# Performance work log

Hardware: AMD Instinct MI355X
Metric: run time of the kernel (lower is better)

## Reference

```python
import jax, jax.numpy as jnp
import numpy as np

H = 256       # hidden_size
W2V = 300     # word embedding dim
POS = 30      # pos embedding dim
NF = 100      # filters per n-gram CNN
VOCAB = 50000
NPOS = 100
N_EDUS = 1024
L = 20        # tokens per EDU


def setup_inputs() -> dict:
    key = jax.random.key(0)
    ks = jax.random.split(key, 22)
    def nrm(k, shape, s=0.05):
        return jax.random.normal(k, shape, dtype=jnp.float32) * s
    cw = W2V + POS  # CNN input width = 330
    # valid transition sequence: S, then (S, R) repeated n-1 times -> 2n-1 steps
    transes = jnp.concatenate([jnp.zeros((1,), jnp.int32),
                               jnp.tile(jnp.array([0, 1], jnp.int32), N_EDUS - 1)])
    return {
        "edu_words": jax.random.randint(ks[0], (N_EDUS, L), 0, VOCAB),
        "edu_poses": jax.random.randint(ks[1], (N_EDUS, L), 0, NPOS),
        "transes": transes,
        "word_emb": nrm(ks[2], (VOCAB, W2V), 1.0),
        "pos_emb": nrm(ks[3], (NPOS, POS), 1.0),
        "Wu": nrm(ks[4], (NF, 1, 1, cw)), "bu": nrm(ks[5], (NF,)),
        "Wb": nrm(ks[6], (NF, 1, 2, cw)), "bb": nrm(ks[7], (NF,)),
        "Wt": nrm(ks[8], (NF, 1, 3, cw)), "bt": nrm(ks[9], (NF,)),
        "Wp": nrm(ks[10], (2 * H, 2 * W2V + POS + 3 * NF)), "bp": nrm(ks[11], (2 * H,)),
        "Wih": nrm(ks[12], (4 * H, 3 * H)), "Whh": nrm(ks[13], (4 * H, H)),
        "bih": nrm(ks[14], (4 * H,)), "bhh": nrm(ks[15], (4 * H,)),
        "Wc": nrm(ks[16], (5 * H, 3 * H)), "bc": nrm(ks[17], (5 * H,)),
        "Ws": nrm(ks[18], (2, H)), "bs": nrm(ks[19], (2,)),
    }


def _encode_edus(edu_words, edu_poses, word_emb, pos_emb, Wu, bu, Wb, bb, Wt, bt, Wp, bp):
    we = word_emb[edu_words]                # [N, L, 300]
    pe = pos_emb[edu_poses]                 # [N, L, 30]
    x = jnp.concatenate([we, pe], axis=-1)[:, None, :, :]  # NCHW [N,1,L,330]
    def conv_pool(W, b, pad):
        # kernel spans full width -> output width 1; pad only along time
        y = jax.lax.conv_general_dilated(x, W, (1, 1), ((pad, pad), (0, 0)),
                                         dimension_numbers=("NCHW", "OIHW", "NCHW"))[..., 0]
        return jax.nn.relu(y + b[None, :, None]).max(axis=-1)  # [N, F]
    feats = jnp.concatenate([we[:, 0], we[:, -1], pe[:, 0],
                             conv_pool(Wu, bu, 0), conv_pool(Wb, bb, 1),
                             conv_pool(Wt, bt, 2)], axis=-1)   # [N, 930]
    h, c = jnp.split(feats @ Wp.T + bp, 2, axis=-1)
    return h, c


def _parse_loss(edu_words, edu_poses, transes, word_emb, pos_emb, Wu, bu, Wb, bb, Wt, bt,
                Wp, bp, Wih, Whh, bih, bhh, Wc, bc, Ws, bs):
    eh, ec = _encode_edus(edu_words, edu_poses, word_emb, pos_emb, Wu, bu, Wb, bb, Wt, bt, Wp, bp)
    M = N_EDUS + 2
    buf_h = jnp.concatenate([eh, jnp.zeros((2, H), jnp.float32)], axis=0)
    buf_c = jnp.concatenate([ec, jnp.zeros((2, H), jnp.float32)], axis=0)
    stack_h = jnp.zeros((M, H), jnp.float32)  # slots 0,1 are the initial placeholders
    stack_c = jnp.zeros((M, H), jnp.float32)

    def lstm(xv, h, c):  # torch LSTMCell gate order i,f,g,o
        g = xv @ Wih.T + bih + h @ Whh.T + bhh
        i, f, gg, o = jnp.split(g, 4)
        c2 = jax.nn.sigmoid(f) * c + jax.nn.sigmoid(i) * jnp.tanh(gg)
        return jax.nn.sigmoid(o) * jnp.tanh(c2), c2

    def track(sh, sptr, bptr, th, tc):
        xv = jnp.concatenate([sh[sptr - 1], sh[sptr - 2], buf_h[bptr]])
        return lstm(xv, th, tc)

    sptr = jnp.int32(2)
    bptr = jnp.int32(0)
    th, tc = track(stack_h, sptr, bptr, jnp.zeros(H, jnp.float32), jnp.zeros(H, jnp.float32))

    def step(carry, trans):
        sh, sc, sptr, bptr, th, tc = carry
        logits = th @ Ws.T + bs  # scorer MLP with mlp_layers=1 -> single Linear
        is_shift = trans == 0
        # SHIFT candidate: push buffer front
        sh_s = sh.at[sptr].set(buf_h[bptr])
        sc_s = sc.at[sptr].set(buf_c[bptr])
        # REDUCE candidate: tree-LSTM composition of top two stack items
        h1, c1 = sh[sptr - 1], sc[sptr - 1]
        h2, c2 = sh[sptr - 2], sc[sptr - 2]
        g = jnp.concatenate([h1, h2, th]) @ Wc.T + bc
        a, i, f1, f2, o = jnp.split(g, 5)
        rc = jnp.tanh(a) * jax.nn.sigmoid(i) + jax.nn.sigmoid(f1) * c1 + jax.nn.sigmoid(f2) * c2
        rh = jax.nn.sigmoid(o) * jnp.tanh(rc)
        sh_r = sh.at[sptr - 2].set(rh)
        sc_r = sc.at[sptr - 2].set(rc)
        sh2 = jnp.where(is_shift, sh_s, sh_r)
        sc2 = jnp.where(is_shift, sc_s, sc_r)
        sptr2 = jnp.where(is_shift, sptr + 1, sptr - 1)
        bptr2 = jnp.where(is_shift, bptr + 1, bptr)
        th2, tc2 = track(sh2, sptr2, bptr2, th, tc)
        return (sh2, sc2, sptr2, bptr2, th2, tc2), logits

    _, pred = jax.lax.scan(step, (stack_h, stack_c, sptr, bptr, th, tc), transes)
    logp = jax.nn.log_softmax(pred, axis=-1)
    return -jnp.mean(logp[jnp.arange(transes.shape[0]), transes])


def reference(edu_words, edu_poses, transes, word_emb, pos_emb, Wu, bu, Wb, bb, Wt, bt,
              Wp, bp, Wih, Whh, bih, bhh, Wc, bc, Ws, bs):
    return _parse_loss(edu_words, edu_poses, transes, word_emb, pos_emb, Wu, bu, Wb, bb,
                       Wt, bt, Wp, bp, Wih, Whh, bih, bhh, Wc, bc, Ws, bs)
```

## Files before the change

kernel.cpp:

```cpp
#include <hip/hip_runtime.h>
#include <math.h>

#define NEDU  1024
#define LTOK  20
#define CW    330
#define HDIM  256
#define FEAT  930
#define MSLOT 1026
#define NWG   64

#define O_WCATT 0
#define SZ_WCATT (330*600)
#define O_F     (O_WCATT + SZ_WCATT)
#define SZ_F    (NEDU*FEAT)
#define O_BUFH  (O_F + SZ_F)
#define SZ_BUF  (MSLOT*HDIM)
#define O_BUFC  (O_BUFH + SZ_BUF)
#define O_STKT  (O_BUFC + SZ_BUF)
#define O_THT   (O_STKT + MSLOT*HDIM)
#define O_RHT   (O_THT + 2*HDIM)
#define O_LOSSP (O_RHT + HDIM)
#define NZERO   ((MSLOT + 3) * HDIM)

#define AG __HIP_MEMORY_SCOPE_AGENT
__device__ __forceinline__ unsigned long long aload64(const unsigned long long* p) {
  return __hip_atomic_load(p, __ATOMIC_RELAXED, AG);
}
__device__ __forceinline__ void astore(unsigned* p, unsigned v) {
  __hip_atomic_store(p, v, __ATOMIC_RELAXED, AG);
}
__device__ __forceinline__ unsigned tagbits(float v, unsigned ver) {
  return (__float_as_uint(v) & ~3u) | (ver & 3u);
}
__device__ __forceinline__ float sigm(float x) { return 1.f / (1.f + expf(-x)); }

__device__ __forceinline__ void sync_lds() {
  asm volatile("s_waitcnt lgkmcnt(0)\n\ts_barrier" ::: "memory");
}

__device__ __forceinline__ void gather1T(const unsigned* base, int lane, unsigned tag,
                                         float* x) {
  const unsigned long long* p = (const unsigned long long*)base + 2 * lane;
  for (int it = 0;; ++it) {
    const unsigned long long a = aload64(p), b = aload64(p + 1);
    const bool ok = (((unsigned)a & 3u) == tag) & (((unsigned)(a >> 32) & 3u) == tag) &
                    (((unsigned)b & 3u) == tag) & (((unsigned)(b >> 32) & 3u) == tag);
    if (__ballot(ok) == ~0ull) {
      x[0] = __uint_as_float((unsigned)a); x[1] = __uint_as_float((unsigned)(a >> 32));
      x[2] = __uint_as_float((unsigned)b); x[3] = __uint_as_float((unsigned)(b >> 32));
      return;
    }
    if (it > 48) __builtin_amdgcn_s_sleep(1);
  }
}
__device__ __forceinline__ void gather2T(const unsigned* b1, unsigned t1,
                                         const unsigned* b2, unsigned t2,
                                         int lane, float* x1, float* x2) {
  const unsigned long long* p1 = (const unsigned long long*)b1 + 2 * lane;
  const unsigned long long* p2 = (const unsigned long long*)b2 + 2 * lane;
  for (int it = 0;; ++it) {
    const unsigned long long a = aload64(p1), b = aload64(p1 + 1);
    const unsigned long long c = aload64(p2), d = aload64(p2 + 1);
    const bool ok = (((unsigned)a & 3u) == t1) & (((unsigned)(a >> 32) & 3u) == t1) &
                    (((unsigned)b & 3u) == t1) & (((unsigned)(b >> 32) & 3u) == t1) &
                    (((unsigned)c & 3u) == t2) & (((unsigned)(c >> 32) & 3u) == t2) &
                    (((unsigned)d & 3u) == t2) & (((unsigned)(d >> 32) & 3u) == t2);
    if (__ballot(ok) == ~0ull) {
      x1[0] = __uint_as_float((unsigned)a); x1[1] = __uint_as_float((unsigned)(a >> 32));
      x1[2] = __uint_as_float((unsigned)b); x1[3] = __uint_as_float((unsigned)(b >> 32));
      x2[0] = __uint_as_float((unsigned)c); x2[1] = __uint_as_float((unsigned)(c >> 32));
      x2[2] = __uint_as_float((unsigned)d); x2[3] = __uint_as_float((unsigned)(d >> 32));
      return;
    }
    if (it > 48) __builtin_amdgcn_s_sleep(1);
  }
}

__global__ void prep_kernel(const float* __restrict__ Wu, const float* __restrict__ Wb,
                            const float* __restrict__ Wt, float* __restrict__ ws) {
  const int i0 = blockIdx.x * blockDim.x + threadIdx.x;
  const int st = gridDim.x * blockDim.x;
  for (int i = i0; i < SZ_WCATT; i += st) {
    const int k = i / 600, c = i - 600 * k;
    float v;
    if (c < 100)      v = Wu[c * 330 + k];
    else if (c < 300) { const int q = c - 100; v = Wb[(q % 100) * 660 + (q / 100) * 330 + k]; }
    else              { const int q = c - 300; v = Wt[(q % 100) * 990 + (q / 100) * 330 + k]; }
    ws[O_WCATT + i] = v;
  }
  unsigned* z = (unsigned*)ws + O_STKT;
  for (int i = i0; i < NZERO; i += st) z[i] = 0u;
  for (int i = i0; i < 2 * HDIM; i += st) {
    ws[O_BUFH + NEDU * HDIM + i] = 0.f;
    ws[O_BUFC + NEDU * HDIM + i] = 0.f;
  }
}

__global__ __launch_bounds__(256) void encode_kernel(
    const int* __restrict__ edu_words, const int* __restrict__ edu_poses,
    const float* __restrict__ word_emb, const float* __restrict__ pos_emb,
    const float* __restrict__ bu, const float* __restrict__ bb,
    const float* __restrict__ bt, float* __restrict__ ws) {
  __shared__ __align__(16) float xlT[CW * LTOK];
  __shared__ float zl[300 * 21];
  __shared__ float convout[300];
  const int n = blockIdx.x, tid = threadIdx.x;
  const float* WcatT = ws + O_WCATT;

  for (int i = tid; i < LTOK * CW; i += 256) {
    const int l = i / CW, k = i - l * CW;
    float v;
    if (k < 300) v = word_emb[(size_t)edu_words[n * LTOK + l] * 300 + k];
    else         v = pos_emb[(size_t)edu_poses[n * LTOK + l] * 30 + (k - 300)];
    xlT[k * LTOK + l] = v;
  }
  __syncthreads();

  for (int f = tid; f < 300; f += 256) {
    float acc[LTOK];
#pragma unroll
    for (int l = 0; l < LTOK; ++l) acc[l] = 0.f;
    for (int k = 0; k < CW; ++k) {
      const float w = WcatT[k * 600 + f];
      const float4* xp = (const float4*)(xlT + k * LTOK);
      union { float4 v[5]; float s[20]; } xu;
      xu.v[0] = xp[0]; xu.v[1] = xp[1]; xu.v[2] = xp[2]; xu.v[3] = xp[3]; xu.v[4] = xp[4];
#pragma unroll
      for (int l = 0; l < LTOK; ++l) acc[l] += w * xu.s[l];
    }
#pragma unroll
    for (int l = 0; l < LTOK; ++l) zl[f * 21 + l] = acc[l];
  }
  __syncthreads();
  if (tid < 200) {
    float m;
    if (tid < 100) {
      const int f = tid; const float b = bu[f];
      m = zl[f * 21] + b;
      for (int l = 1; l < 20; ++l) m = fmaxf(m, zl[f * 21 + l] + b);
    } else {
      const int f = tid - 100; const float b = bb[f];
      const float* z0 = zl + (100 + f) * 21;
      const float* z1 = zl + (200 + f) * 21;
      m = z1[0] + b;
      for (int u = 1; u <= 19; ++u) m = fmaxf(m, z0[u - 1] + z1[u] + b);
      m = fmaxf(m, z0[19] + b);
    }
    convout[tid] = fmaxf(m, 0.f);
  }
  __syncthreads();

  for (int f = tid; f < 300; f += 256) {
    float acc[LTOK];
#pragma unroll
    for (int l = 0; l < LTOK; ++l) acc[l] = 0.f;
    for (int k = 0; k < CW; ++k) {
      const float w = WcatT[k * 600 + 300 + f];
      const float4* xp = (const float4*)(xlT + k * LTOK);
      union { float4 v[5]; float s[20]; } xu;
      xu.v[0] = xp[0]; xu.v[1] = xp[1]; xu.v[2] = xp[2]; xu.v[3] = xp[3]; xu.v[4] = xp[4];
#pragma unroll
      for (int l = 0; l < LTOK; ++l) acc[l] += w * xu.s[l];
    }
#pragma unroll
    for (int l = 0; l < LTOK; ++l) zl[f * 21 + l] = acc[l];
  }
  __syncthreads();
  if (tid < 100) {
    const int f = tid; const float b = bt[f];
    const float* z0 = zl + f * 21;
    const float* z1 = zl + (100 + f) * 21;
    const float* z2 = zl + (200 + f) * 21;
    float m = z2[0] + b;
    m = fmaxf(m, z1[0] + z2[1] + b);
    for (int u = 2; u <= 19; ++u) m = fmaxf(m, z0[u - 2] + z1[u - 1] + z2[u] + b);
    m = fmaxf(m, z0[18] + z1[19] + b);
    m = fmaxf(m, z0[19] + b);
    convout[200 + f] = fmaxf(m, 0.f);
  }
  __syncthreads();

  float* Fr = ws + O_F + (size_t)n * FEAT;
  for (int j = tid; j < FEAT; j += 256) {
    float v;
    if (j < 300)      v = xlT[j * LTOK + 0];
    else if (j < 600) v = xlT[(j - 300) * LTOK + 19];
    else if (j < 630) v = xlT[(j - 300) * LTOK + 0];
    else              v = convout[j - 630];
    Fr[j] = v;
  }
}

__global__ __launch_bounds__(256) void proj_kernel(const float* __restrict__ Wp,
                                                   const float* __restrict__ bp,
                                                   float* __restrict__ ws) {
  __shared__ float As[64][17];
  __shared__ float Bs[64][17];
  const float* F = ws + O_F;
  float* bufh = ws + O_BUFH;
  float* bufc = ws + O_BUFC;
  const int tid = threadIdx.x;
  const int m0 = blockIdx.x * 64, n0 = blockIdx.y * 64;
  const int mm0 = (tid & 15) * 4, nn0 = (tid >> 4) * 4;
  float acc[4][4] = {{0.f}};
  for (int k0 = 0; k0 < FEAT; k0 += 16) {
    for (int i = tid; i < 64 * 16; i += 256) {
      const int mm = i >> 4, kk = i & 15;
      const int gk = k0 + kk;
      As[mm][kk] = (gk < FEAT) ? F[(size_t)(m0 + mm) * FEAT + gk] : 0.f;
      Bs[mm][kk] = (gk < FEAT) ? Wp[(size_t)(n0 + mm) * FEAT + gk] : 0.f;
    }
    __syncthreads();
#pragma unroll
    for (int kk = 0; kk < 16; ++kk) {
      float av[4], bv[4];
#pragma unroll
      for (int i = 0; i < 4; ++i) av[i] = As[mm0 + i][kk];
#pragma unroll
      for (int j = 0; j < 4; ++j) bv[j] = Bs[nn0 + j][kk];
#pragma unroll
      for (int i = 0; i < 4; ++i)
#pragma unroll
        for (int j = 0; j < 4; ++j) acc[i][j] += av[i] * bv[j];
    }
    __syncthreads();
  }
#pragma unroll
  for (int i = 0; i < 4; ++i) {
    const int m = m0 + mm0 + i;
#pragma unroll
    for (int j = 0; j < 4; ++j) {
      const int nn = n0 + nn0 + j;
      const float v = acc[i][j] + bp[nn];
      if (nn < 256) bufh[(size_t)m * 256 + nn] = v;
      else          bufc[(size_t)m * 256 + (nn - 256)] = v;
    }
  }
}

__global__ __launch_bounds__(256, 1) void parse_kernel(
    const int* __restrict__ transes, int nT,
    const float* __restrict__ Wih, const float* __restrict__ Whh,
    const float* __restrict__ bih, const float* __restrict__ bhh,
    const float* __restrict__ Wc, const float* __restrict__ bc,
    const float* __restrict__ Wsc, float* __restrict__ ws) {
  const int tid = threadIdx.x;
  const int lane = tid & 63;
  const int wv = tid >> 6;
  const int bx = blockIdx.x;
  const int j0 = bx * 4;

  const float* bufh = ws + O_BUFH;
  const float* bufc = ws + O_BUFC;
  unsigned* stkT = (unsigned*)ws + O_STKT;
  unsigned* thT  = (unsigned*)ws + O_THT;
  unsigned* rhT  = (unsigned*)ws + O_RHT;
  float* lossp   = ws + O_LOSSP;

  __shared__ float sc_lds[MSLOT][4];
  __shared__ unsigned vstk[MSLOT];
  __shared__ float tc_lds[2][4];
  __shared__ float g_lds[20];
  __shared__ float rh_st[4];
  __shared__ float part_lds[8];

  float wt[4][16]; float bt_[4];
#pragma unroll
  for (int q = 0; q < 4; ++q) {
    const int rg = wv * 256 + j0 + q;
#pragma unroll
    for (int blk = 0; blk < 3; ++blk) {
      const float4 w = *(const float4*)(Wih + (size_t)rg * 768 + blk * 256 + 4 * lane);
      wt[q][4 * blk + 0] = w.x; wt[q][4 * blk + 1] = w.y;
      wt[q][4 * blk + 2] = w.z; wt[q][4 * blk + 3] = w.w;
    }
    const float4 wh = *(const float4*)(Whh + (size_t)rg * 256 + 4 * lane);
    wt[q][12] = wh.x; wt[q][13] = wh.y; wt[q][14] = wh.z; wt[q][15] = wh.w;
    bt_[q] = bih[rg] + bhh[rg];
  }
  float wcm[5][12]; float bc_[5];
#pragma unroll
  for (int q = 0; q < 5; ++q) {
    const int row = 5 * wv + q, gate = row >> 2, jj = row & 3;
    const int rg = gate * 256 + j0 + jj;
#pragma unroll
    for (int blk = 0; blk < 3; ++blk) {
      const float4 w = *(const float4*)(Wc + (size_t)rg * 768 + blk * 256 + 4 * lane);
      wcm[q][4 * blk + 0] = w.x; wcm[q][4 * blk + 1] = w.y;
      wcm[q][4 * blk + 2] = w.z; wcm[q][4 * blk + 3] = w.w;
    }
    bc_[q] = bc[rg];
  }
  float ws0 = 0.f, ws1 = 0.f;
  if (tid < 4) { ws0 = Wsc[j0 + tid]; ws1 = Wsc[256 + j0 + tid]; }

  for (int i = tid; i < MSLOT; i += 256) vstk[i] = 0u;
  if (tid < 4) { sc_lds[0][tid] = 0.f; sc_lds[1][tid] = 0.f;
                 tc_lds[0][tid] = 0.f; tc_lds[1][tid] = 0.f; }
  __syncthreads();

  unsigned V = 0, vrh = 0;
  int sptr = 2, bptr = 0;

  auto red4 = [&](float& a0, float& a1, float& a2, float& a3) {
#pragma unroll
    for (int off = 32; off; off >>= 1) {
      a0 += __shfl_down(a0, off, 64); a1 += __shfl_down(a1, off, 64);
      a2 += __shfl_down(a2, off, 64); a3 += __shfl_down(a3, off, 64);
    }
  };
  auto red5 = [&](float& a0, float& a1, float& a2, float& a3, float& a4) {
#pragma unroll
    for (int off = 32; off; off >>= 1) {
      a0 += __shfl_down(a0, off, 64); a1 += __shfl_down(a1, off, 64);
      a2 += __shfl_down(a2, off, 64); a3 += __shfl_down(a3, off, 64);
      a4 += __shfl_down(a4, off, 64);
    }
  };

  auto fin_track = [&]() {
    const int j = j0 + tid;
    const float gi = g_lds[tid], gf = g_lds[4 + tid], gg = g_lds[8 + tid], go = g_lds[12 + tid];
    const float cn = sigm(gf) * tc_lds[V & 1][tid] + sigm(gi) * tanhf(gg);
    tc_lds[(V + 1) & 1][tid] = cn;
    const float th = sigm(go) * tanhf(cn);
    astore(thT + ((V + 1) & 1) * HDIM + j, tagbits(th, V + 1));
    part_lds[tid] = ws0 * th; part_lds[4 + tid] = ws1 * th;
  };
  auto emit_loss = [&]() {
    float* lp = lossp + (size_t)V * 128 + bx * 2;
    lp[0] = part_lds[0] + part_lds[1] + part_lds[2] + part_lds[3];
    lp[1] = part_lds[4] + part_lds[5] + part_lds[6] + part_lds[7];
  };
  auto dyn_track = [&](const unsigned* fbase, unsigned ftag, int fblk,
                       float s0, float s1, float s2, float s3) {
    float x[4];
    gather1T(fbase, lane, ftag, x);
    float d0 = 0.f, d1 = 0.f, d2 = 0.f, d3 = 0.f;
#pragma unroll
    for (int c = 0; c < 4; ++c) {
      d0 += wt[0][4 * fblk + c] * x[c]; d1 += wt[1][4 * fblk + c] * x[c];
      d2 += wt[2][4 * fblk + c] * x[c]; d3 += wt[3][4 * fblk + c] * x[c];
    }
    red4(d0, d1, d2, d3);
    if (lane == 0) {
      g_lds[wv * 4 + 0] = s0 + d0 + bt_[0]; g_lds[wv * 4 + 1] = s1 + d1 + bt_[1];
      g_lds[wv * 4 + 2] = s2 + d2 + bt_[2]; g_lds[wv * 4 + 3] = s3 + d3 + bt_[3];
    }
    sync_lds();
    if (tid < 4) fin_track();
    if (tid == 0) emit_loss();
  };

  {
    float p1[4], p2[4];
    gather2T(stkT + HDIM, 0u, stkT, 0u, lane, p1, p2);
    const float4 f3 = *(const float4*)(bufh + 4 * lane);
    const float p3[4] = { f3.x, f3.y, f3.z, f3.w };
    float s0 = 0.f, s1 = 0.f, s2 = 0.f, s3 = 0.f;
#pragma unroll
    for (int c = 0; c < 4; ++c) {
      s0 += wt[0][c] * p1[c] + wt[0][4 + c] * p2[c] + wt[0][8 + c] * p3[c];
      s1 += wt[1][c] * p1[c] + wt[1][4 + c] * p2[c] + wt[1][8 + c] * p3[c];
      s2 += wt[2][c] * p1[c] + wt[2][4 + c] * p2[c] + wt[2][8 + c] * p3[c];
      s3 += wt[3][c] * p1[c] + wt[3][4 + c] * p2[c] + wt[3][8 + c] * p3[c];
    }
    red4(s0, s1, s2, s3);
    dyn_track(thT + (V & 1) * HDIM, V & 3, 3, s0, s1, s2, s3);
    sync_lds();
    V += 1;
  }

  for (int t = 0; t < nT; ++t) {
    const int tr = transes[t];
    if (tr) {
      {
        float h1[4], h2[4];
        gather2T(stkT + (size_t)(sptr - 1) * HDIM, vstk[sptr - 1] & 3,
                 stkT + (size_t)(sptr - 2) * HDIM, vstk[sptr - 2] & 3, lane, h1, h2);
        float s0 = 0.f, s1 = 0.f, s2 = 0.f, s3 = 0.f, s4 = 0.f;
#pragma unroll
        for (int c = 0; c < 4; ++c) {
          s0 += wcm[0][c] * h1[c] + wcm[0][4 + c] * h2[c];
          s1 += wcm[1][c] * h1[c] + wcm[1][4 + c] * h2[c];
          s2 += wcm[2][c] * h1[c] + wcm[2][4 + c] * h2[c];
          s3 += wcm[3][c] * h1[c] + wcm[3][4 + c] * h2[c];
          s4 += wcm[4][c] * h1[c] + wcm[4][4 + c] * h2[c];
        }
        red5(s0, s1, s2, s3, s4);
        float x[4];
        gather1T(thT + (V & 1) * HDIM, lane, V & 3, x);
        float d0 = 0.f, d1 = 0.f, d2 = 0.f, d3 = 0.f, d4 = 0.f;
#pragma unroll
        for (int c = 0; c < 4; ++c) {
          d0 += wcm[0][8 + c] * x[c]; d1 += wcm[1][8 + c] * x[c];
          d2 += wcm[2][8 + c] * x[c]; d3 += wcm[3][8 + c] * x[c];
          d4 += wcm[4][8 + c] * x[c];
        }
        red5(d0, d1, d2, d3, d4);
        if (lane == 0) {
          g_lds[5 * wv + 0] = s0 + d0 + bc_[0]; g_lds[5 * wv + 1] = s1 + d1 + bc_[1];
          g_lds[5 * wv + 2] = s2 + d2 + bc_[2]; g_lds[5 * wv + 3] = s3 + d3 + bc_[3];
          g_lds[5 * wv + 4] = s4 + d4 + bc_[4];
        }
      }
      sync_lds();
      if (tid < 4) {
        const int j = j0 + tid;
        const float ga = g_lds[tid], gi = g_lds[4 + tid], gf1 = g_lds[8 + tid],
                    gf2 = g_lds[12 + tid], go = g_lds[16 + tid];
        const float c1 = sc_lds[sptr - 1][tid];
        const float c2 = sc_lds[sptr - 2][tid];
        const float rc = tanhf(ga) * sigm(gi) + sigm(gf1) * c1 + sigm(gf2) * c2;
        const float rh = sigm(go) * tanhf(rc);
        sc_lds[sptr - 2][tid] = rc;
        rh_st[tid] = rh;
        astore(rhT + j, tagbits(rh, vrh + 1));
      }
      sync_lds();
      vrh += 1;

      {
        const int slot = sptr - 2;
        const unsigned nv = vstk[slot] + 1;
        if (tid < 4)
          astore(stkT + (size_t)slot * HDIM + j0 + tid, tagbits(rh_st[tid], nv));
        float p2[4], xth[4];
        gather2T(stkT + (size_t)(sptr - 3) * HDIM, vstk[sptr - 3] & 3,
                 thT + (V & 1) * HDIM, V & 3, lane, p2, xth);
        const float4 f3 = *(const float4*)(bufh + (size_t)bptr * HDIM + 4 * lane);
        const float p3[4] = { f3.x, f3.y, f3.z, f3.w };
        float s0 = 0.f, s1 = 0.f, s2 = 0.f, s3 = 0.f;
#pragma unroll
        for (int c = 0; c < 4; ++c) {
          s0 += wt[0][4 + c] * p2[c] + wt[0][8 + c] * p3[c] + wt[0][12 + c] * xth[c];
          s1 += wt[1][4 + c] * p2[c] + wt[1][8 + c] * p3[c] + wt[1][12 + c] * xth[c];
          s2 += wt[2][4 + c] * p2[c] + wt[2][8 + c] * p3[c] + wt[2][12 + c] * xth[c];
          s3 += wt[3][4 + c] * p2[c] + wt[3][8 + c] * p3[c] + wt[3][12 + c] * xth[c];
        }
        red4(s0, s1, s2, s3);
        dyn_track(rhT, vrh & 3, 0, s0, s1, s2, s3);
        if (tid == 0) vstk[slot] = nv;
        sync_lds();
        V += 1; sptr -= 1;
      }
    } else {
      const unsigned nv = vstk[sptr] + 1;
      if (tid < 4) {
        const int j = j0 + tid;
        astore(stkT + (size_t)sptr * HDIM + j, tagbits(bufh[(size_t)bptr * HDIM + j], nv));
        sc_lds[sptr][tid] = bufc[(size_t)bptr * HDIM + j];
      }
      const float4 f1 = *(const float4*)(bufh + (size_t)bptr * HDIM + 4 * lane);
      const float4 f3 = *(const float4*)(bufh + (size_t)(bptr + 1) * HDIM + 4 * lane);
      float p2[4];
      gather1T(stkT + (size_t)(sptr - 1) * HDIM, lane, vstk[sptr - 1] & 3, p2);
      const float p1[4] = { f1.x, f1.y, f1.z, f1.w };
      const float p3[4] = { f3.x, f3.y, f3.z, f3.w };
      float s0 = 0.f, s1 = 0.f, s2 = 0.f, s3 = 0.f;
#pragma unroll
      for (int c = 0; c < 4; ++c) {
        s0 += wt[0][c] * p1[c] + wt[0][4 + c] * p2[c] + wt[0][8 + c] * p3[c];
        s1 += wt[1][c] * p1[c] + wt[1][4 + c] * p2[c] + wt[1][8 + c] * p3[c];
        s2 += wt[2][c] * p1[c] + wt[2][4 + c] * p2[c] + wt[2][8 + c] * p3[c];
        s3 += wt[3][c] * p1[c] + wt[3][4 + c] * p2[c] + wt[3][8 + c] * p3[c];
      }
      red4(s0, s1, s2, s3);
      dyn_track(thT + (V & 1) * HDIM, V & 3, 3, s0, s1, s2, s3);
      if (tid == 0) vstk[sptr] = nv;
      sync_lds();
      V += 1; sptr += 1; bptr += 1;
    }
  }
}

__global__ __launch_bounds__(256) void loss_kernel(const int* __restrict__ transes, int nT,
                                                   const float* __restrict__ bsc,
                                                   const float* __restrict__ ws,
                                                   float* __restrict__ out) {
  const int tid = threadIdx.x;
  const float* lossp = ws + O_LOSSP;
  __shared__ double red[256];
  double acc = 0.0;
  for (int t = tid; t < nT; t += 256) {
    const float* lp = lossp + (size_t)t * 128;
    float a0 = 0.f, a1 = 0.f;
    for (int w = 0; w < 64; ++w) { a0 += lp[2 * w]; a1 += lp[2 * w + 1]; }
    const float l0 = a0 + bsc[0], l1 = a1 + bsc[1];
    const float mx = fmaxf(l0, l1);
    acc += (double)(mx + logf(expf(l0 - mx) + expf(l1 - mx)) - (transes[t] ? l1 : l0));
  }
  red[tid] = acc;
  __syncthreads();
  for (int s = 128; s; s >>= 1) {
    if (tid < s) red[tid] += red[tid + s];
    __syncthreads();
  }
  if (tid == 0) out[0] = (float)(red[0] / (double)nT);
}

extern "C" void kernel_launch(void* const* d_in, const int* in_sizes, int n_in,
                              void* d_out, int out_size, void* d_ws, size_t ws_size,
                              hipStream_t stream) {
  const int*   edu_words = (const int*)d_in[0];
  const int*   edu_poses = (const int*)d_in[1];
  const int*   transes   = (const int*)d_in[2];
  const float* word_emb  = (const float*)d_in[3];
  const float* pos_emb   = (const float*)d_in[4];
  const float* Wu  = (const float*)d_in[5];
  const float* bu  = (const float*)d_in[6];
  const float* Wb  = (const float*)d_in[7];
  const float* bb  = (const float*)d_in[8];
  const float* Wt  = (const float*)d_in[9];
  const float* bt  = (const float*)d_in[10];
  const float* Wp  = (const float*)d_in[11];
  const float* bp  = (const float*)d_in[12];
  const float* Wih = (const float*)d_in[13];
  const float* Whh = (const float*)d_in[14];
  const float* bih = (const float*)d_in[15];
  const float* bhh = (const float*)d_in[16];
  const float* Wc  = (const float*)d_in[17];
  const float* bc  = (const float*)d_in[18];
  const float* Wsc = (const float*)d_in[19];
  const float* bsc = (const float*)d_in[20];
  float* ws  = (float*)d_ws;
  float* out = (float*)d_out;
  int nT = in_sizes[2];

  hipLaunchKernelGGL(prep_kernel, dim3(256), dim3(256), 0, stream, Wu, Wb, Wt, ws);
  hipLaunchKernelGGL(encode_kernel, dim3(NEDU), dim3(256), 0, stream,
                     edu_words, edu_poses, word_emb, pos_emb, bu, bb, bt, ws);
  hipLaunchKernelGGL(proj_kernel, dim3(16, 8), dim3(256), 0, stream, Wp, bp, ws);

  void* args[] = { (void*)&transes, (void*)&nT, (void*)&Wih, (void*)&Whh, (void*)&bih,
                   (void*)&bhh, (void*)&Wc, (void*)&bc, (void*)&Wsc, (void*)&ws };
  hipLaunchCooperativeKernel((const void*)parse_kernel, dim3(NWG), dim3(256), args, 0, stream);

  hipLaunchKernelGGL(loss_kernel, dim3(1), dim3(256), 0, stream, transes, nT, bsc, ws, out);
}
```

Baseline: 7.515 ms.

## Make each wavefront own one hidden unit, removing intra-block barriers in parse loop

After: 13.01 ms. 73.1% more time.

```diff
diff --git a/kernel.cpp b/kernel.cpp
--- a/kernel.cpp
+++ b/kernel.cpp
@@ -9,21 +9,25 @@
 #define MSLOT 1026
 #define NWG   64
 
+typedef unsigned long long u64;
+
 #define O_WCATT 0
 #define SZ_WCATT (330*600)
 #define O_F     (O_WCATT + SZ_WCATT)
 #define SZ_F    (NEDU*FEAT)
-#define O_BUFH  (O_F + SZ_F)
+#define O_LOSSP O_F
+#define SZ_LOSSP (2048*512)
+#define SZ_FL   1048576
+#define O_BUFH  (O_F + SZ_FL)
 #define SZ_BUF  (MSLOT*HDIM)
 #define O_BUFC  (O_BUFH + SZ_BUF)
 #define O_STKT  (O_BUFC + SZ_BUF)
 #define O_THT   (O_STKT + MSLOT*HDIM)
 #define O_RHT   (O_THT + 2*HDIM)
-#define O_LOSSP (O_RHT + HDIM)
 #define NZERO   ((MSLOT + 3) * HDIM)
 
 #define AG __HIP_MEMORY_SCOPE_AGENT
-__device__ __forceinline__ unsigned long long aload64(const unsigned long long* p) {
+__device__ __forceinline__ u64 aload64(const u64* p) {
   return __hip_atomic_load(p, __ATOMIC_RELAXED, AG);
 }
 __device__ __forceinline__ void astore(unsigned* p, unsigned v) {
@@ -32,47 +36,47 @@
 __device__ __forceinline__ unsigned tagbits(float v, unsigned ver) {
   return (__float_as_uint(v) & ~3u) | (ver & 3u);
 }
-__device__ __forceinline__ float sigm(float x) { return 1.f / (1.f + expf(-x)); }
-
-__device__ __forceinline__ void sync_lds() {
-  asm volatile("s_waitcnt lgkmcnt(0)\n\ts_barrier" ::: "memory");
-}
-
-__device__ __forceinline__ void gather1T(const unsigned* base, int lane, unsigned tag,
-                                         float* x) {
-  const unsigned long long* p = (const unsigned long long*)base + 2 * lane;
+__device__ __forceinline__ bool tagok(u64 v, unsigned tag) {
+  return (((unsigned)v & 3u) == tag) & (((unsigned)(v >> 32) & 3u) == tag);
+}
+__device__ __forceinline__ float sigm_f(float x) { return 1.f / (1.f + __expf(-x)); }
+__device__ __forceinline__ float tanh_f(float x) {
+  const float xc = fminf(fmaxf(x, -15.f), 15.f);
+  const float e = __expf(2.f * xc);
+  return (e - 1.f) / (e + 1.f);
+}
+__device__ __forceinline__ void unpack(u64 a, u64 b, float* x) {
+  x[0] = __uint_as_float((unsigned)a); x[1] = __uint_as_float((unsigned)(a >> 32));
+  x[2] = __uint_as_float((unsigned)b); x[3] = __uint_as_float((unsigned)(b >> 32));
+}
+__device__ __forceinline__ void gather2(const unsigned* b1, unsigned t1,
+                                        const unsigned* b2, unsigned t2,
+                                        int lane, float* x1, float* x2) {
+  const u64* p1 = (const u64*)b1 + 2 * lane;
+  const u64* p2 = (const u64*)b2 + 2 * lane;
   for (int it = 0;; ++it) {
-    const unsigned long long a = aload64(p), b = aload64(p + 1);
-    const bool ok = (((unsigned)a & 3u) == tag) & (((unsigned)(a >> 32) & 3u) == tag) &
-                    (((unsigned)b & 3u) == tag) & (((unsigned)(b >> 32) & 3u) == tag);
-    if (__ballot(ok) == ~0ull) {
-      x[0] = __uint_as_float((unsigned)a); x[1] = __uint_as_float((unsigned)(a >> 32));
-      x[2] = __uint_as_float((unsigned)b); x[3] = __uint_as_float((unsigned)(b >> 32));
-      return;
-    }
-    if (it > 48) __builtin_amdgcn_s_sleep(1);
-  }
-}
-__device__ __forceinline__ void gather2T(const unsigned* b1, unsigned t1,
-                                         const unsigned* b2, unsigned t2,
-                                         int lane, float* x1, float* x2) {
-  const unsigned long long* p1 = (const unsigned long long*)b1 + 2 * lane;
-  const unsigned long long* p2 = (const unsigned long long*)b2 + 2 * lane;
+    const u64 a = aload64(p1), b = aload64(p1 + 1);
+    const u64 c = aload64(p2), d = aload64(p2 + 1);
+    const bool ok = tagok(a, t1) & tagok(b, t1) & tagok(c, t2) & tagok(d, t2);
+    if (__ballot(ok) == ~0ull) { unpack(a, b, x1); unpack(c, d, x2); return; }
+    if (it > 32) __builtin_amdgcn_s_sleep(1);
+  }
+}
+__device__ __forceinline__ void gather3(const unsigned* b1, unsigned t1,
+                                        const unsigned* b2, unsigned t2,
+                                        const unsigned* b3, unsigned t3,
+                                        int lane, float* x1, float* x2, float* x3) {
+  const u64* p1 = (const u64*)b1 + 2 * lane;
+  const u64* p2 = (const u64*)b2 + 2 * lane;
+  const u64* p3 = (const u64*)b3 + 2 * lane;
   for (int it = 0;; ++it) {
-    const unsigned long long a = aload64(p1), b = aload64(p1 + 1);
-    const unsigned long long c = aload64(p2), d = aload64(p2 + 1);
-    const bool ok = (((unsigned)a & 3u) == t1) & (((unsigned)(a >> 32) & 3u) == t1) &
-                    (((unsigned)b & 3u) == t1) & (((unsigned)(b >> 32) & 3u) == t1) &
-                    (((unsigned)c & 3u) == t2) & (((unsigned)(c >> 32) & 3u) == t2) &
-                    (((unsigned)d & 3u) == t2) & (((unsigned)(d >> 32) & 3u) == t2);
-    if (__ballot(ok) == ~0ull) {
-      x1[0] = __uint_as_float((unsigned)a); x1[1] = __uint_as_float((unsigned)(a >> 32));
-      x1[2] = __uint_as_float((unsigned)b); x1[3] = __uint_as_float((unsigned)(b >> 32));
-      x2[0] = __uint_as_float((unsigned)c); x2[1] = __uint_as_float((unsigned)(c >> 32));
-      x2[2] = __uint_as_float((unsigned)d); x2[3] = __uint_as_float((unsigned)(d >> 32));
-      return;
-    }
-    if (it > 48) __builtin_amdgcn_s_sleep(1);
+    const u64 a = aload64(p1), b = aload64(p1 + 1);
+    const u64 c = aload64(p2), d = aload64(p2 + 1);
+    const u64 e = aload64(p3), f = aload64(p3 + 1);
+    const bool ok = tagok(a, t1) & tagok(b, t1) & tagok(c, t2) & tagok(d, t2) &
+                    tagok(e, t3) & tagok(f, t3);
+    if (__ballot(ok) == ~0ull) { unpack(a, b, x1); unpack(c, d, x2); unpack(e, f, x3); return; }
+    if (it > 32) __builtin_amdgcn_s_sleep(1);
   }
 }
 
@@ -246,9 +250,8 @@
     const float* __restrict__ Wsc, float* __restrict__ ws) {
   const int tid = threadIdx.x;
   const int lane = tid & 63;
-  const int wv = tid >> 6;
-  const int bx = blockIdx.x;
-  const int j0 = bx * 4;
+  const int wv  = tid >> 6;
+  const int j   = blockIdx.x * 4 + wv;
 
   const float* bufh = ws + O_BUFH;
   const float* bufc = ws + O_BUFC;
@@ -257,50 +260,45 @@
   unsigned* rhT  = (unsigned*)ws + O_RHT;
   float* lossp   = ws + O_LOSSP;
 
-  __shared__ float sc_lds[MSLOT][4];
-  __shared__ unsigned vstk[MSLOT];
-  __shared__ float tc_lds[2][4];
-  __shared__ float g_lds[20];
-  __shared__ float rh_st[4];
-  __shared__ float part_lds[8];
+  __shared__ float    sc_lds[MSLOT][4];
+  __shared__ unsigned vstk[4][MSLOT];
 
   float wt[4][16]; float bt_[4];
 #pragma unroll
-  for (int q = 0; q < 4; ++q) {
-    const int rg = wv * 256 + j0 + q;
+  for (int g = 0; g < 4; ++g) {
+    const int rg = g * 256 + j;
 #pragma unroll
     for (int blk = 0; blk < 3; ++blk) {
       const float4 w = *(const float4*)(Wih + (size_t)rg * 768 + blk * 256 + 4 * lane);
-      wt[q][4 * blk + 0] = w.x; wt[q][4 * blk + 1] = w.y;
-      wt[q][4 * blk + 2] = w.z; wt[q][4 * blk + 3] = w.w;
+      wt[g][4 * blk + 0] = w.x; wt[g][4 * blk + 1] = w.y;
+      wt[g][4 * blk + 2] = w.z; wt[g][4 * blk + 3] = w.w;
     }
     const float4 wh = *(const float4*)(Whh + (size_t)rg * 256 + 4 * lane);
-    wt[q][12] = wh.x; wt[q][13] = wh.y; wt[q][14] = wh.z; wt[q][15] = wh.w;
-    bt_[q] = bih[rg] + bhh[rg];
+    wt[g][12] = wh.x; wt[g][13] = wh.y; wt[g][14] = wh.z; wt[g][15] = wh.w;
+    bt_[g] = bih[rg] + bhh[rg];
   }
   float wcm[5][12]; float bc_[5];
 #pragma unroll
-  for (int q = 0; q < 5; ++q) {
-    const int row = 5 * wv + q, gate = row >> 2, jj = row & 3;
-    const int rg = gate * 256 + j0 + jj;
+  for (int g = 0; g < 5; ++g) {
+    const int rg = g * 256 + j;
 #pragma unroll
     for (int blk = 0; blk < 3; ++blk) {
       const float4 w = *(const float4*)(Wc + (size_t)rg * 768 + blk * 256 + 4 * lane);
-      wcm[q][4 * blk + 0] = w.x; wcm[q][4 * blk + 1] = w.y;
-      wcm[q][4 * blk + 2] = w.z; wcm[q][4 * blk + 3] = w.w;
-    }
-    bc_[q] = bc[rg];
-  }
-  float ws0 = 0.f, ws1 = 0.f;
-  if (tid < 4) { ws0 = Wsc[j0 + tid]; ws1 = Wsc[256 + j0 + tid]; }
-
-  for (int i = tid; i < MSLOT; i += 256) vstk[i] = 0u;
-  if (tid < 4) { sc_lds[0][tid] = 0.f; sc_lds[1][tid] = 0.f;
-                 tc_lds[0][tid] = 0.f; tc_lds[1][tid] = 0.f; }
+      wcm[g][4 * blk + 0] = w.x; wcm[g][4 * blk + 1] = w.y;
+      wcm[g][4 * blk + 2] = w.z; wcm[g][4 * blk + 3] = w.w;
+    }
+    bc_[g] = bc[rg];
+  }
+  const float ws0 = Wsc[j], ws1 = Wsc[256 + j];
+
+  for (int i = tid; i < 4 * MSLOT; i += 256) (&vstk[0][0])[i] = 0u;
+  if (lane == 0) { sc_lds[0][wv] = 0.f; sc_lds[1][wv] = 0.f; }
   __syncthreads();
 
   unsigned V = 0, vrh = 0;
   int sptr = 2, bptr = 0;
+  float tc_reg = 0.f, rh_reg = 0.f;
+  float xth[4];
 
   auto red4 = [&](float& a0, float& a1, float& a2, float& a3) {
 #pragma unroll
@@ -318,57 +316,34 @@
     }
   };
 
-  auto fin_track = [&]() {
-    const int j = j0 + tid;
-    const float gi = g_lds[tid], gf = g_lds[4 + tid], gg = g_lds[8 + tid], go = g_lds[12 + tid];
-    const float cn = sigm(gf) * tc_lds[V & 1][tid] + sigm(gi) * tanhf(gg);
-    tc_lds[(V + 1) & 1][tid] = cn;
-    const float th = sigm(go) * tanhf(cn);
-    astore(thT + ((V + 1) & 1) * HDIM + j, tagbits(th, V + 1));
-    part_lds[tid] = ws0 * th; part_lds[4 + tid] = ws1 * th;
+  auto fin_track = [&](float d0, float d1, float d2, float d3) {
+    if (lane == 0) {
+      const float gi = d0 + bt_[0], gf = d1 + bt_[1], gg = d2 + bt_[2], go = d3 + bt_[3];
+      const float cn = sigm_f(gf) * tc_reg + sigm_f(gi) * tanh_f(gg);
+      tc_reg = cn;
+      const float th = sigm_f(go) * tanh_f(cn);
+      astore(thT + ((V + 1) & 1) * HDIM + j, tagbits(th, V + 1));
+      float* lp = lossp + (size_t)V * 512 + 2 * j;
+      lp[0] = ws0 * th; lp[1] = ws1 * th;
+    }
+    V += 1;
   };
-  auto emit_loss = [&]() {
-    float* lp = lossp + (size_t)V * 128 + bx * 2;
-    lp[0] = part_lds[0] + part_lds[1] + part_lds[2] + part_lds[3];
-    lp[1] = part_lds[4] + part_lds[5] + part_lds[6] + part_lds[7];
-  };
-  auto dyn_track = [&](const unsigned* fbase, unsigned ftag, int fblk,
-                       float s0, float s1, float s2, float s3) {
-    float x[4];
-    gather1T(fbase, lane, ftag, x);
+
+  {
+    const float4 f3 = *(const float4*)(bufh + 4 * lane);
+    float p1[4], p2[4], xf[4];
+    gather3(stkT + HDIM, 0u, stkT, 0u, thT, 0u, lane, p1, p2, xf);
     float d0 = 0.f, d1 = 0.f, d2 = 0.f, d3 = 0.f;
+    const float p3[4] = { f3.x, f3.y, f3.z, f3.w };
 #pragma unroll
     for (int c = 0; c < 4; ++c) {
-      d0 += wt[0][4 * fblk + c] * x[c]; d1 += wt[1][4 * fblk + c] * x[c];
-      d2 += wt[2][4 * fblk + c] * x[c]; d3 += wt[3][4 * fblk + c] * x[c];
+      d0 += wt[0][c]*p1[c] + wt[0][4+c]*p2[c] + wt[0][8+c]*p3[c] + wt[0][12+c]*xf[c];
+      d1 += wt[1][c]*p1[c] + wt[1][4+c]*p2[c] + wt[1][8+c]*p3[c] + wt[1][12+c]*xf[c];
+      d2 += wt[2][c]*p1[c] + wt[2][4+c]*p2[c] + wt[2][8+c]*p3[c] + wt[2][12+c]*xf[c];
+      d3 += wt[3][c]*p1[c] + wt[3][4+c]*p2[c] + wt[3][8+c]*p3[c] + wt[3][12+c]*xf[c];
     }
     red4(d0, d1, d2, d3);
-    if (lane == 0) {
-      g_lds[wv * 4 + 0] = s0 + d0 + bt_[0]; g_lds[wv * 4 + 1] = s1 + d1 + bt_[1];
-      g_lds[wv * 4 + 2] = s2 + d2 + bt_[2]; g_lds[wv * 4 + 3] = s3 + d3 + bt_[3];
-    }
-    sync_lds();
-    if (tid < 4) fin_track();
-    if (tid == 0) emit_loss();
-  };
-
-  {
-    float p1[4], p2[4];
-    gather2T(stkT + HDIM, 0u, stkT, 0u, lane, p1, p2);
-    const float4 f3 = *(const float4*)(bufh + 4 * lane);
-    const float p3[4] = { f3.x, f3.y, f3.z, f3.w };
-    float s0 = 0.f, s1 = 0.f, s2 = 0.f, s3 = 0.f;
-#pragma unroll
-    for (int c = 0; c < 4; ++c) {
-      s0 += wt[0][c] * p1[c] + wt[0][4 + c] * p2[c] + wt[0][8 + c] * p3[c];
-      s1 += wt[1][c] * p1[c] + wt[1][4 + c] * p2[c] + wt[1][8 + c] * p3[c];
-      s2 += wt[2][c] * p1[c] + wt[2][4 + c] * p2[c] + wt[2][8 + c] * p3[c];
-      s3 += wt[3][c] * p1[c] + wt[3][4 + c] * p2[c] + wt[3][8 + c] * p3[c];
-    }
-    red4(s0, s1, s2, s3);
-    dyn_track(thT + (V & 1) * HDIM, V & 3, 3, s0, s1, s2, s3);
-    sync_lds();
-    V += 1;
+    fin_track(d0, d1, d2, d3);
   }
 
   for (int t = 0; t < nT; ++t) {
@@ -376,100 +351,80 @@
     if (tr) {
       {
         float h1[4], h2[4];
-        gather2T(stkT + (size_t)(sptr - 1) * HDIM, vstk[sptr - 1] & 3,
-                 stkT + (size_t)(sptr - 2) * HDIM, vstk[sptr - 2] & 3, lane, h1, h2);
-        float s0 = 0.f, s1 = 0.f, s2 = 0.f, s3 = 0.f, s4 = 0.f;
+        gather3(stkT + (size_t)(sptr - 1) * HDIM, vstk[wv][sptr - 1] & 3,
+                stkT + (size_t)(sptr - 2) * HDIM, vstk[wv][sptr - 2] & 3,
+                thT + (V & 1) * HDIM, V & 3, lane, h1, h2, xth);
+        float e0 = 0.f, e1 = 0.f, e2 = 0.f, e3 = 0.f, e4 = 0.f;
 #pragma unroll
         for (int c = 0; c < 4; ++c) {
-          s0 += wcm[0][c] * h1[c] + wcm[0][4 + c] * h2[c];
-          s1 += wcm[1][c] * h1[c] + wcm[1][4 + c] * h2[c];
-          s2 += wcm[2][c] * h1[c] + wcm[2][4 + c] * h2[c];
-          s3 += wcm[3][c] * h1[c] + wcm[3][4 + c] * h2[c];
-          s4 += wcm[4][c] * h1[c] + wcm[4][4 + c] * h2[c];
+          e0 += wcm[0][c]*h1[c] + wcm[0][4+c]*h2[c] + wcm[0][8+c]*xth[c];
+          e1 += wcm[1][c]*h1[c] + wcm[1][4+c]*h2[c] + wcm[1][8+c]*xth[c];
+          e2 += wcm[2][c]*h1[c] + wcm[2][4+c]*h2[c] + wcm[2][8+c]*xth[c];
+          e3 += wcm[3][c]*h1[c] + wcm[3][4+c]*h2[c] + wcm[3][8+c]*xth[c];
+          e4 += wcm[4][c]*h1[c] + wcm[4][4+c]*h2[c] + wcm[4][8+c]*xth[c];
         }
-        red5(s0, s1, s2, s3, s4);
-        float x[4];
-        gather1T(thT + (V & 1) * HDIM, lane, V & 3, x);
-        float d0 = 0.f, d1 = 0.f, d2 = 0.f, d3 = 0.f, d4 = 0.f;
+        red5(e0, e1, e2, e3, e4);
+        if (lane == 0) {
+          const float ga = e0 + bc_[0], gi = e1 + bc_[1], gf1 = e2 + bc_[2],
+                      gf2 = e3 + bc_[3], go = e4 + bc_[4];
+          const float c1 = sc_lds[sptr - 1][wv];
+          const float c2 = sc_lds[sptr - 2][wv];
+          const float rc = tanh_f(ga) * sigm_f(gi) + sigm_f(gf1) * c1 + sigm_f(gf2) * c2;
+          sc_lds[sptr - 2][wv] = rc;
+          rh_reg = sigm_f(go) * tanh_f(rc);
+          astore(rhT + j, tagbits(rh_reg, vrh + 1));
+        }
+        vrh += 1;
+      }
+      {
+        const float4 f3 = *(const float4*)(bufh + (size_t)bptr * HDIM + 4 * lane);
+        float pr[4], p2[4];
+        gather2(rhT, vrh & 3,
+                stkT + (size_t)(sptr - 3) * HDIM, vstk[wv][sptr - 3] & 3, lane, pr, p2);
+        const unsigned nv2 = vstk[wv][sptr - 2] + 1;
+        __atomic_signal_fence(__ATOMIC_SEQ_CST);
+        if (lane == 0) {
+          astore(stkT + (size_t)(sptr - 2) * HDIM + j, tagbits(rh_reg, nv2));
+          vstk[wv][sptr - 2] = nv2;
+        }
+        const float p3[4] = { f3.x, f3.y, f3.z, f3.w };
+        float d0 = 0.f, d1 = 0.f, d2 = 0.f, d3 = 0.f;
 #pragma unroll
         for (int c = 0; c < 4; ++c) {
-          d0 += wcm[0][8 + c] * x[c]; d1 += wcm[1][8 + c] * x[c];
-          d2 += wcm[2][8 + c] * x[c]; d3 += wcm[3][8 + c] * x[c];
-          d4 += wcm[4][8 + c] * x[c];
+          d0 += wt[0][c]*pr[c] + wt[0][4+c]*p2[c] + wt[0][8+c]*p3[c] + wt[0][12+c]*xth[c];
+          d1 += wt[1][c]*pr[c] + wt[1][4+c]*p2[c] + wt[1][8+c]*p3[c] + wt[1][12+c]*xth[c];
+          d2 += wt[2][c]*pr[c] + wt[2][4+c]*p2[c] + wt[2][8+c]*p3[c] + wt[2][12+c]*xth[c];
+          d3 += wt[3][c]*pr[c] + wt[3][4+c]*p2[c] + wt[3][8+c]*p3[c] + wt[3][12+c]*xth[c];
         }
-        red5(d0, d1, d2, d3, d4);
-        if (lane == 0) {
-          g_lds[5 * wv + 0] = s0 + d0 + bc_[0]; g_lds[5 * wv + 1] = s1 + d1 + bc_[1];
-          g_lds[5 * wv + 2] = s2 + d2 + bc_[2]; g_lds[5 * wv + 3] = s3 + d3 + bc_[3];
-          g_lds[5 * wv + 4] = s4 + d4 + bc_[4];
-        }
-      }
-      sync_lds();
-      if (tid < 4) {
-        const int j = j0 + tid;
-        const float ga = g_lds[tid], gi = g_lds[4 + tid], gf1 = g_lds[8 + tid],
-                    gf2 = g_lds[12 + tid], go = g_lds[16 + tid];
-        const float c1 = sc_lds[sptr - 1][tid];
-        const float c2 = sc_lds[sptr - 2][tid];
-        const float rc = tanhf(ga) * sigm(gi) + sigm(gf1) * c1 + sigm(gf2) * c2;
-        const float rh = sigm(go) * tanhf(rc);
-        sc_lds[sptr - 2][tid] = rc;
-        rh_st[tid] = rh;
-        astore(rhT + j, tagbits(rh, vrh + 1));
-      }
-      sync_lds();
-      vrh += 1;
-
-      {
-        const int slot = sptr - 2;
-        const unsigned nv = vstk[slot] + 1;
-        if (tid < 4)
-          astore(stkT + (size_t)slot * HDIM + j0 + tid, tagbits(rh_st[tid], nv));
-        float p2[4], xth[4];
-        gather2T(stkT + (size_t)(sptr - 3) * HDIM, vstk[sptr - 3] & 3,
-                 thT + (V & 1) * HDIM, V & 3, lane, p2, xth);
-        const float4 f3 = *(const float4*)(bufh + (size_t)bptr * HDIM + 4 * lane);
-        const float p3[4] = { f3.x, f3.y, f3.z, f3.w };
-        float s0 = 0.f, s1 = 0.f, s2 = 0.f, s3 = 0.f;
-#pragma unroll
-        for (int c = 0; c < 4; ++c) {
-          s0 += wt[0][4 + c] * p2[c] + wt[0][8 + c] * p3[c] + wt[0][12 + c] * xth[c];
-          s1 += wt[1][4 + c] * p2[c] + wt[1][8 + c] * p3[c] + wt[1][12 + c] * xth[c];
-          s2 += wt[2][4 + c] * p2[c] + wt[2][8 + c] * p3[c] + wt[2][12 + c] * xth[c];
-          s3 += wt[3][4 + c] * p2[c] + wt[3][8 + c] * p3[c] + wt[3][12 + c] * xth[c];
-        }
-        red4(s0, s1, s2, s3);
-        dyn_track(rhT, vrh & 3, 0, s0, s1, s2, s3);
-        if (tid == 0) vstk[slot] = nv;
-        sync_lds();
-        V += 1; sptr -= 1;
+        red4(d0, d1, d2, d3);
+        fin_track(d0, d1, d2, d3);
+        sptr -= 1;
       }
     } else {
-      const unsigned nv = vstk[sptr] + 1;
-      if (tid < 4) {
-        const int j = j0 + tid;
+      const unsigned nv = vstk[wv][sptr] + 1;
+      if (lane == 0) {
         astore(stkT + (size_t)sptr * HDIM + j, tagbits(bufh[(size_t)bptr * HDIM + j], nv));
-        sc_lds[sptr][tid] = bufc[(size_t)bptr * HDIM + j];
+        sc_lds[sptr][wv] = bufc[(size_t)bptr * HDIM + j];
+        vstk[wv][sptr] = nv;
       }
       const float4 f1 = *(const float4*)(bufh + (size_t)bptr * HDIM + 4 * lane);
       const float4 f3 = *(const float4*)(bufh + (size_t)(bptr + 1) * HDIM + 4 * lane);
-      float p2[4];
-      gather1T(stkT + (size_t)(sptr - 1) * HDIM, lane, vstk[sptr - 1] & 3, p2);
+      float p2[4], xf[4];
+      gather2(stkT + (size_t)(sptr - 1) * HDIM, vstk[wv][sptr - 1] & 3,
+              thT + (V & 1) * HDIM, V & 3, lane, p2, xf);
       const float p1[4] = { f1.x, f1.y, f1.z, f1.w };
       const float p3[4] = { f3.x, f3.y, f3.z, f3.w };
-      float s0 = 0.f, s1 = 0.f, s2 = 0.f, s3 = 0.f;
+      float d0 = 0.f, d1 = 0.f, d2 = 0.f, d3 = 0.f;
 #pragma unroll
       for (int c = 0; c < 4; ++c) {
-        s0 += wt[0][c] * p1[c] + wt[0][4 + c] * p2[c] + wt[0][8 + c] * p3[c];
-        s1 += wt[1][c] * p1[c] + wt[1][4 + c] * p2[c] + wt[1][8 + c] * p3[c];
-        s2 += wt[2][c] * p1[c] + wt[2][4 + c] * p2[c] + wt[2][8 + c] * p3[c];
-        s3 += wt[3][c] * p1[c] + wt[3][4 + c] * p2[c] + wt[3][8 + c] * p3[c];
+        d0 += wt[0][c]*p1[c] + wt[0][4+c]*p2[c] + wt[0][8+c]*p3[c] + wt[0][12+c]*xf[c];
+        d1 += wt[1][c]*p1[c] + wt[1][4+c]*p2[c] + wt[1][8+c]*p3[c] + wt[1][12+c]*xf[c];
+        d2 += wt[2][c]*p1[c] + wt[2][4+c]*p2[c] + wt[2][8+c]*p3[c] + wt[2][12+c]*xf[c];
+        d3 += wt[3][c]*p1[c] + wt[3][4+c]*p2[c] + wt[3][8+c]*p3[c] + wt[3][12+c]*xf[c];
       }
-      red4(s0, s1, s2, s3);
-      dyn_track(thT + (V & 1) * HDIM, V & 3, 3, s0, s1, s2, s3);
-      if (tid == 0) vstk[sptr] = nv;
-      sync_lds();
-      V += 1; sptr += 1; bptr += 1;
+      red4(d0, d1, d2, d3);
+      fin_track(d0, d1, d2, d3);
+      sptr += 1; bptr += 1;
     }
   }
 }
@@ -483,9 +438,9 @@
   __shared__ double red[256];
   double acc = 0.0;
   for (int t = tid; t < nT; t += 256) {
-    const float* lp = lossp + (size_t)t * 128;
+    const float2* lp = (const float2*)(lossp + (size_t)t * 512);
     float a0 = 0.f, a1 = 0.f;
-    for (int w = 0; w < 64; ++w) { a0 += lp[2 * w]; a1 += lp[2 * w + 1]; }
+    for (int k = 0; k < 256; ++k) { const float2 v = lp[k]; a0 += v.x; a1 += v.y; }
     const float l0 = a0 + bsc[0], l1 = a1 + bsc[1];
     const float mx = fmaxf(l0, l1);
     acc += (double)(mx + logf(expf(l0 - mx) + expf(l1 - mx)) - (transes[t] ? l1 : l0));
```
